# Kernel optimization log

Hardware: AMD Instinct MI355X
Metric: run time of the kernel (lower is better)

Reference implementation:

```python
import math
import jax, jax.numpy as jnp
import numpy as np

D = 256      # embedding_dim (= internal_dim, downsample_rate 1)
H = 8        # num_heads
HD = D // H  # head_dim = 32
NTC = 16     # num_text_classes
NIMG = 4096  # image tokens (64x64)
N = NIMG + NTC
B = 2
NKE = 64     # num_k_exclude_rope


def _rope(x, freqs):
    # x: (b, h, n, c); freqs: (n, c//2, 2) = (cos, sin) of complex rotary factors
    b, h, n, c = x.shape
    xp = x.reshape(b, h, n, c // 2, 2)
    cos, sin = freqs[..., 0], freqs[..., 1]
    xr, xi = xp[..., 0], xp[..., 1]
    out_r = xr * cos - xi * sin
    out_i = xr * sin + xi * cos
    return jnp.stack([out_r, out_i], axis=-1).reshape(b, h, n, c)


def _sep_heads(x):
    b, n, c = x.shape
    return x.reshape(b, n, H, c // H).transpose(0, 2, 1, 3)  # (b,h,n,hd)


def setup_inputs() -> dict:
    key = jax.random.key(0)
    ks = jax.random.split(key, 14)
    s = 0.02
    # rotary factors: unit-norm cos/sin pairs
    ang_img = jax.random.uniform(ks[3], (NIMG, HD // 2)) * (2.0 * np.pi)
    ang_txt = jax.random.uniform(ks[4], (NTC, HD // 2)) * (2.0 * np.pi)
    return {
        "q": jax.random.normal(ks[0], (B, N, D), dtype=jnp.float32),
        "k": jax.random.normal(ks[1], (B, N, D), dtype=jnp.float32),
        "v": jax.random.normal(ks[2], (B, N, D), dtype=jnp.float32),
        "freqs_cis_img": jnp.stack([jnp.cos(ang_img), jnp.sin(ang_img)], axis=-1),
        "freqs_cis_txt": jnp.stack([jnp.cos(ang_txt), jnp.sin(ang_txt)], axis=-1),
        "Wq": jax.random.normal(ks[5], (D, D), dtype=jnp.float32) * s,
        "bq": jnp.zeros((D,), dtype=jnp.float32),
        "Wk": jax.random.normal(ks[6], (D, D), dtype=jnp.float32) * s,
        "bk": jnp.zeros((D,), dtype=jnp.float32),
        "Wv": jax.random.normal(ks[7], (D, D), dtype=jnp.float32) * s,
        "bv": jnp.zeros((D,), dtype=jnp.float32),
        "Wo": jax.random.normal(ks[8], (D, D), dtype=jnp.float32) * s,
        "bo": jnp.zeros((D,), dtype=jnp.float32),
        "num_k_exclude_rope": NKE,
    }


def reference(q, k, v, freqs_cis_img, freqs_cis_txt,
              Wq, bq, Wk, bk, Wv, bv, Wo, bo, num_k_exclude_rope):
    q = q @ Wq.T + bq
    k = k @ Wk.T + bk
    v = v @ Wv.T + bv
    q = _sep_heads(q)  # (b,h,n,hd)
    k = _sep_heads(k)
    v = _sep_heads(v)

    # split tokens into image / text regions, apply RoPE separately
    q_img, q_txt = q[:, :, :-NTC, :], q[:, :, -NTC:, :]
    k_img, k_txt = k[:, :, :-NTC, :], k[:, :, -NTC:, :]
    q_img = _rope(q_img, freqs_cis_img)
    k_img = _rope(k_img, freqs_cis_img)
    q_txt = _rope(q_txt, freqs_cis_txt)
    k_txt = _rope(k_txt, freqs_cis_txt)
    q = jnp.concatenate([q_img, q_txt], axis=-2)
    k = jnp.concatenate([k_img, k_txt], axis=-2)

    scale = 1.0 / math.sqrt(HD)
    nke = num_k_exclude_rope
    if nke > 0:
        k_td, k_mem = k[:, :, :-nke, :], k[:, :, -nke:, :]
        v_td, v_mem = v[:, :, :-nke, :], v[:, :, -nke:, :]
        attn = jax.nn.softmax(jnp.einsum('bhqd,bhkd->bhqk', q, k_td) * scale, axis=-1)
        out = jnp.einsum('bhqk,bhkd->bhqd', attn, v_td)
        attn_m = jax.nn.softmax(jnp.einsum('bhqd,bhkd->bhqk', q, k_mem) * scale, axis=-1)
        out = out + jnp.einsum('bhqk,bhkd->bhqd', attn_m, v_mem)
    else:
        attn = jax.nn.softmax(jnp.einsum('bhqd,bhkd->bhqk', q, k) * scale, axis=-1)
        out = jnp.einsum('bhqk,bhkd->bhqd', attn, v)

    b, h, n, hd = out.shape
    out = out.transpose(0, 2, 1, 3).reshape(b, n, h * hd)
    return out @ Wo.T + bo
```

## Files before the change

kernel.cpp:

```cpp
#include <hip/hip_runtime.h>
#include <hip/hip_bf16.h>

#define BN    4112
#define NKR   4160
#define BNP   4160
#define BB    2
#define HH    8
#define NIMG_ 4096
#define NMAIN 4048
#define MROWS 8224
#define QSCALE 0.25505402f

typedef __attribute__((ext_vector_type(8))) short short8;
typedef __attribute__((ext_vector_type(4))) float f32x4;

__device__ __forceinline__ unsigned short f2bs(float x) { return __bfloat16_as_ushort(__float2bfloat16(x)); }
__device__ __forceinline__ unsigned pkbf(float a, float b) {
    __hip_bfloat162 h = __float22bfloat162_rn(make_float2(a, b));
    unsigned u; __builtin_memcpy(&u, &h, 4); return u;
}
__device__ __forceinline__ float fexp2(float x) {
#if __has_builtin(__builtin_amdgcn_exp2f)
    return __builtin_amdgcn_exp2f(x);
#else
    return exp2f(x);
#endif
}

__global__ __launch_bounds__(256)
void qkv_mfma(const float* __restrict__ Aq, const float* __restrict__ Ak, const float* __restrict__ Av,
              const float* __restrict__ Wq, const float* __restrict__ Wk, const float* __restrict__ Wv,
              const float* __restrict__ bq, const float* __restrict__ bk, const float* __restrict__ bv,
              short* __restrict__ Qr, short* __restrict__ Kr, short* __restrict__ Vt,
              const float* __restrict__ fimg, const float* __restrict__ ftxt)
{
    __shared__ __align__(16) short Ws[2][64][72];
    __shared__ __align__(16) short Ds[2][64][72];

    const int mode = blockIdx.z;
    const float* A    = (mode == 0) ? Aq : (mode == 1) ? Ak : Av;
    const float* W    = (mode == 0) ? Wq : (mode == 1) ? Wk : Wv;
    const float* bias = (mode == 0) ? bq : (mode == 1) ? bk : bv;

    const int t    = threadIdx.x;
    const int wave = t >> 6, lane = t & 63, q16 = lane & 15, quad = lane >> 4;
    const int f0 = blockIdx.x * 64;
    const int m0 = blockIdx.y * 64;
    const int sr = t >> 2, sc = (t & 3) * 16;
    const int arow = m0 + sr;
    const bool aval = arow < MROWS;
    const float* wp = W + (size_t)(f0 + sr) * 256 + sc;
    const float* ap = A + (size_t)(aval ? arow : 0) * 256 + sc;

    f32x4 acc[4] = {{0,0,0,0},{0,0,0,0},{0,0,0,0},{0,0,0,0}};

    uint4 wr0, wr1, dr0, dr1;
    {
        float4 a0 = *(const float4*)(wp),     a1 = *(const float4*)(wp + 4);
        float4 a2 = *(const float4*)(wp + 8), a3 = *(const float4*)(wp + 12);
        wr0 = uint4{pkbf(a0.x,a0.y), pkbf(a0.z,a0.w), pkbf(a1.x,a1.y), pkbf(a1.z,a1.w)};
        wr1 = uint4{pkbf(a2.x,a2.y), pkbf(a2.z,a2.w), pkbf(a3.x,a3.y), pkbf(a3.z,a3.w)};
        a0 = *(const float4*)(ap);     a1 = *(const float4*)(ap + 4);
        a2 = *(const float4*)(ap + 8); a3 = *(const float4*)(ap + 12);
        dr0 = uint4{pkbf(a0.x,a0.y), pkbf(a0.z,a0.w), pkbf(a1.x,a1.y), pkbf(a1.z,a1.w)};
        dr1 = uint4{pkbf(a2.x,a2.y), pkbf(a2.z,a2.w), pkbf(a3.x,a3.y), pkbf(a3.z,a3.w)};
    }
    *(uint4*)&Ws[0][sr][sc] = wr0; *(uint4*)&Ws[0][sr][sc + 8] = wr1;
    *(uint4*)&Ds[0][sr][sc] = dr0; *(uint4*)&Ds[0][sr][sc + 8] = dr1;
    __syncthreads();

    #pragma unroll
    for (int ki = 0; ki < 4; ++ki) {
        const int buf = ki & 1;
        if (ki < 3) {
            const int k1 = (ki + 1) * 64;
            float4 a0 = *(const float4*)(wp + k1),     a1 = *(const float4*)(wp + k1 + 4);
            float4 a2 = *(const float4*)(wp + k1 + 8), a3 = *(const float4*)(wp + k1 + 12);
            wr0 = uint4{pkbf(a0.x,a0.y), pkbf(a0.z,a0.w), pkbf(a1.x,a1.y), pkbf(a1.z,a1.w)};
            wr1 = uint4{pkbf(a2.x,a2.y), pkbf(a2.z,a2.w), pkbf(a3.x,a3.y), pkbf(a3.z,a3.w)};
            a0 = *(const float4*)(ap + k1);     a1 = *(const float4*)(ap + k1 + 4);
            a2 = *(const float4*)(ap + k1 + 8); a3 = *(const float4*)(ap + k1 + 12);
            dr0 = uint4{pkbf(a0.x,a0.y), pkbf(a0.z,a0.w), pkbf(a1.x,a1.y), pkbf(a1.z,a1.w)};
            dr1 = uint4{pkbf(a2.x,a2.y), pkbf(a2.z,a2.w), pkbf(a3.x,a3.y), pkbf(a3.z,a3.w)};
        }
        #pragma unroll
        for (int ks = 0; ks < 2; ++ks) {
            const short8 af = *(const short8*)&Ws[buf][wave * 16 + q16][ks * 32 + quad * 8];
            #pragma unroll
            for (int ct = 0; ct < 4; ++ct) {
                const short8 bf = *(const short8*)&Ds[buf][ct * 16 + q16][ks * 32 + quad * 8];
                acc[ct] = __builtin_amdgcn_mfma_f32_16x16x32_bf16(af, bf, acc[ct], 0, 0, 0);
            }
        }
        if (ki < 3) {
            *(uint4*)&Ws[buf ^ 1][sr][sc] = wr0; *(uint4*)&Ws[buf ^ 1][sr][sc + 8] = wr1;
            *(uint4*)&Ds[buf ^ 1][sr][sc] = dr0; *(uint4*)&Ds[buf ^ 1][sr][sc + 8] = dr1;
            __syncthreads();
        }
    }

    const int fbase = f0 + wave * 16 + quad * 4;
    const float4 bb = *(const float4*)(bias + fbase);
    float vs[4][4];
    #pragma unroll
    for (int ct = 0; ct < 4; ++ct) {
        int n = m0 + ct * 16 + q16;
        float v0 = acc[ct][0] + bb.x, v1 = acc[ct][1] + bb.y;
        float v2 = acc[ct][2] + bb.z, v3 = acc[ct][3] + bb.w;
        int b  = (n >= BN) ? 1 : 0;
        int nb = n - b * BN;
        if (mode < 2) {
            int j0 = (fbase & 31) >> 1;
            const float* fr = (nb < NIMG_) ? (fimg + ((size_t)nb * 16 + j0) * 2)
                                           : (ftxt + ((size_t)(nb - NIMG_) * 16 + j0) * 2);
            float4 cs = *(const float4*)fr;
            float r0 = v0 * cs.x - v1 * cs.y, i0 = v0 * cs.y + v1 * cs.x;
            float r1 = v2 * cs.z - v3 * cs.w, i1 = v2 * cs.w + v3 * cs.z;
            v0 = r0; v1 = i0; v2 = r1; v3 = i1;
        }
        if (mode == 2) {
            vs[ct][0] = v0; vs[ct][1] = v1; vs[ct][2] = v2; vs[ct][3] = v3;
            continue;
        }
        if (n >= MROWS) continue;
        const int h = (fbase >> 5) & 7, hd = fbase & 31;
        if (mode == 0) {
            unsigned short* op = (unsigned short*)Qr + (((size_t)(b * HH + h) * BN + nb) * 32 + hd);
            *(uint2*)op = uint2{pkbf(v0 * QSCALE, v1 * QSCALE), pkbf(v2 * QSCALE, v3 * QSCALE)};
        } else {
            int nk = nb + ((nb >= NMAIN) ? 48 : 0);
            unsigned short* op = (unsigned short*)Kr + (((size_t)(b * HH + h) * NKR + nk) * 32 + hd);
            *(uint2*)op = uint2{pkbf(v0, v1), pkbf(v2, v3)};
        }
    }

    if (mode == 2) {
        short (*Tr)[72] = Ds[0];
        const int fl = wave * 16 + quad * 4;
        #pragma unroll
        for (int ct = 0; ct < 4; ++ct) {
            const int nl = ct * 16 + q16;
            Tr[fl + 0][nl] = (short)f2bs(vs[ct][0]);
            Tr[fl + 1][nl] = (short)f2bs(vs[ct][1]);
            Tr[fl + 2][nl] = (short)f2bs(vs[ct][2]);
            Tr[fl + 3][nl] = (short)f2bs(vs[ct][3]);
        }
        __syncthreads();
        const int h0 = (f0 >> 5) & 7;
        #pragma unroll
        for (int ii = 0; ii < 2; ++ii) {
            const int r  = ii * 32 + (t >> 3);
            const int c8 = (t & 7) * 8;
            const int ng = m0 + c8;
            if (ng < MROWS) {
                uint4 val = *(const uint4*)&Tr[r][c8];
                int b  = (ng >= BN) ? 1 : 0;
                int nb = ng - b * BN;
                int nk = nb + ((nb >= NMAIN) ? 48 : 0);
                int h  = h0 + (r >> 5), hd = r & 31;
                unsigned short* op = (unsigned short*)Vt + ((size_t)(b * HH + h) * 32 + hd) * BNP + nk;
                *(uint4*)op = val;
            }
        }
    }

    if (blockIdx.x == 0 && blockIdx.y < 16 && t < 192) {
        const int bh = blockIdx.y;
        if (mode == 1) {
            short* base = Kr + (size_t)bh * NKR * 32 + (size_t)NMAIN * 32;
            *(uint4*)(base + t * 8) = uint4{0u, 0u, 0u, 0u};
        } else if (mode == 2) {
            short* base = Vt + (size_t)bh * 32 * BNP + (size_t)(t / 6) * BNP + NMAIN + (t % 6) * 8;
            *(uint4*)base = uint4{0u, 0u, 0u, 0u};
        }
    }
}

__global__ __launch_bounds__(256)
void attn_mfma(const short* __restrict__ Qr, const short* __restrict__ Kr,
               const short* __restrict__ Vt, unsigned short* __restrict__ AO)
{
    __shared__ __align__(16) short Ks[2][64][40];
    __shared__ __align__(16) short Vs[2][32][72];

    const int t    = threadIdx.x;
    const int wave = t >> 6, lane = t & 63, q16 = lane & 15, quad = lane >> 4;
    const int bh = blockIdx.y;
    const int q  = blockIdx.x * 64 + wave * 16 + q16;
    const int qc = (q < BN) ? q : (BN - 1);
    const short8 qf = *(const short8*)(Qr + ((size_t)bh * BN + qc) * 32 + quad * 8);

    f32x4 oA0 = {0,0,0,0}, oA1 = {0,0,0,0}, oB0 = {0,0,0,0}, oB1 = {0,0,0,0};
    float LA = 0.f, LB = 0.f;

    const int kr = t >> 2, kc = t & 3;
    const int vr = t >> 3, vc = t & 7;
    const short* kg = Kr + (size_t)bh * NKR * 32 + (size_t)kr * 32 + kc * 8;
    const short* vg = Vt + (size_t)bh * 32 * BNP + (size_t)vr * BNP + vc * 8;

    auto tile = [&](int buf, f32x4& o0, f32x4& o1, float& L) {
        float lsum = 0.f;
        #pragma unroll
        for (int g = 0; g < 2; ++g) {
            const short8 kf0 = *(const short8*)&Ks[buf][(2*g)     * 16 + q16][quad * 8];
            const short8 kf1 = *(const short8*)&Ks[buf][(2*g + 1) * 16 + q16][quad * 8];
            f32x4 z = {0,0,0,0};
            f32x4 s0 = __builtin_amdgcn_mfma_f32_16x16x32_bf16(kf0, qf, z, 0, 0, 0);
            f32x4 s1 = __builtin_amdgcn_mfma_f32_16x16x32_bf16(kf1, qf, z, 0, 0, 0);
            float p0 = fexp2(s0[0]), p1 = fexp2(s0[1]), p2 = fexp2(s0[2]), p3 = fexp2(s0[3]);
            float p4 = fexp2(s1[0]), p5 = fexp2(s1[1]), p6 = fexp2(s1[2]), p7 = fexp2(s1[3]);
            lsum += ((p0 + p1) + (p2 + p3)) + ((p4 + p5) + (p6 + p7));
            uint4 pbu = uint4{pkbf(p0, p1), pkbf(p2, p3), pkbf(p4, p5), pkbf(p6, p7)};
            short8 pb; __builtin_memcpy(&pb, &pbu, 16);
            uint2 va0 = uint2{*(const unsigned*)&Vs[buf][q16][g*32 + quad*4],
                              *(const unsigned*)&Vs[buf][q16][g*32 + quad*4 + 2]};
            uint2 va1 = uint2{*(const unsigned*)&Vs[buf][q16][g*32 + 16 + quad*4],
                              *(const unsigned*)&Vs[buf][q16][g*32 + 16 + quad*4 + 2]};
            uint4 vau = uint4{va0.x, va0.y, va1.x, va1.y};
            short8 vf; __builtin_memcpy(&vf, &vau, 16);
            o0 = __builtin_amdgcn_mfma_f32_16x16x32_bf16(vf, pb, o0, 0, 0, 0);
            uint2 vb0 = uint2{*(const unsigned*)&Vs[buf][16 + q16][g*32 + quad*4],
                              *(const unsigned*)&Vs[buf][16 + q16][g*32 + quad*4 + 2]};
            uint2 vb1 = uint2{*(const unsigned*)&Vs[buf][16 + q16][g*32 + 16 + quad*4],
                              *(const unsigned*)&Vs[buf][16 + q16][g*32 + 16 + quad*4 + 2]};
            uint4 vbu = uint4{vb0.x, vb0.y, vb1.x, vb1.y};
            short8 vg2; __builtin_memcpy(&vg2, &vbu, 16);
            o1 = __builtin_amdgcn_mfma_f32_16x16x32_bf16(vg2, pb, o1, 0, 0, 0);
        }
        L += lsum;
    };

    *(uint4*)&Ks[0][kr][kc * 8] = *(const uint4*)(kg);
    *(uint4*)&Vs[0][vr][vc * 8] = *(const uint4*)(vg);
    __syncthreads();

    for (int it = 0; it < 64; ++it) {
        const int buf = it & 1;
        uint4 kreg = *(const uint4*)(kg + (size_t)(it + 1) * 2048);
        uint4 vreg = *(const uint4*)(vg + (it + 1) * 64);
        tile(buf, oA0, oA1, LA);
        *(uint4*)&Ks[buf ^ 1][kr][kc * 8] = kreg;
        *(uint4*)&Vs[buf ^ 1][vr][vc * 8] = vreg;
        __syncthreads();
    }
    tile(0, oB0, oB1, LB);

    LA += __shfl_xor(LA, 16); LA += __shfl_xor(LA, 32);
    LB += __shfl_xor(LB, 16); LB += __shfl_xor(LB, 32);
    LA -= 48.f;

    if (q < BN) {
        const float iA = 1.f / LA, iB = 1.f / LB;
        const int b = bh >> 3, h = bh & 7;
        unsigned short* ap = AO + ((size_t)b * BN + q) * 256 + h * 32;
        float w0[4], w1[4];
        #pragma unroll
        for (int r = 0; r < 4; ++r) {
            w0[r] = oA0[r] * iA + oB0[r] * iB;
            w1[r] = oA1[r] * iA + oB1[r] * iB;
        }
        *(uint2*)(ap + quad * 4)      = uint2{pkbf(w0[0], w0[1]), pkbf(w0[2], w0[3])};
        *(uint2*)(ap + 16 + quad * 4) = uint2{pkbf(w1[0], w1[1]), pkbf(w1[2], w1[3])};
    }
}

__global__ __launch_bounds__(256)
void gemm_out(const unsigned short* __restrict__ A, const float* __restrict__ W,
              const float* __restrict__ bias, float* __restrict__ out)
{
    __shared__ __align__(16) short Ws[2][64][72];
    __shared__ __align__(16) short Ds[2][64][72];
    const int t    = threadIdx.x;
    const int wave = t >> 6, lane = t & 63, q16 = lane & 15, quad = lane >> 4;
    const int f0 = blockIdx.x * 64, m0 = blockIdx.y * 64;
    const int sr = t >> 2, sc = (t & 3) * 16;
    const int arow = m0 + sr;
    const bool aval = arow < MROWS;
    const float* wp = W + (size_t)(f0 + sr) * 256 + sc;
    const unsigned short* ap = A + (size_t)(aval ? arow : 0) * 256 + sc;

    f32x4 acc[4] = {{0,0,0,0},{0,0,0,0},{0,0,0,0},{0,0,0,0}};

    uint4 wr0, wr1, dr0, dr1;
    {
        float4 a0 = *(const float4*)(wp),     a1 = *(const float4*)(wp + 4);
        float4 a2 = *(const float4*)(wp + 8), a3 = *(const float4*)(wp + 12);
        wr0 = uint4{pkbf(a0.x,a0.y), pkbf(a0.z,a0.w), pkbf(a1.x,a1.y), pkbf(a1.z,a1.w)};
        wr1 = uint4{pkbf(a2.x,a2.y), pkbf(a2.z,a2.w), pkbf(a3.x,a3.y), pkbf(a3.z,a3.w)};
        dr0 = *(const uint4*)(ap); dr1 = *(const uint4*)(ap + 8);
    }
    *(uint4*)&Ws[0][sr][sc] = wr0; *(uint4*)&Ws[0][sr][sc + 8] = wr1;
    *(uint4*)&Ds[0][sr][sc] = dr0; *(uint4*)&Ds[0][sr][sc + 8] = dr1;
    __syncthreads();

    #pragma unroll
    for (int ki = 0; ki < 4; ++ki) {
        const int buf = ki & 1;
        if (ki < 3) {
            const int k1 = (ki + 1) * 64;
            float4 a0 = *(const float4*)(wp + k1),     a1 = *(const float4*)(wp + k1 + 4);
            float4 a2 = *(const float4*)(wp + k1 + 8), a3 = *(const float4*)(wp + k1 + 12);
            wr0 = uint4{pkbf(a0.x,a0.y), pkbf(a0.z,a0.w), pkbf(a1.x,a1.y), pkbf(a1.z,a1.w)};
            wr1 = uint4{pkbf(a2.x,a2.y), pkbf(a2.z,a2.w), pkbf(a3.x,a3.y), pkbf(a3.z,a3.w)};
            dr0 = *(const uint4*)(ap + k1); dr1 = *(const uint4*)(ap + k1 + 8);
        }
        #pragma unroll
        for (int ks = 0; ks < 2; ++ks) {
            const short8 af = *(const short8*)&Ws[buf][wave * 16 + q16][ks * 32 + quad * 8];
            #pragma unroll
            for (int ct = 0; ct < 4; ++ct) {
                const short8 bf = *(const short8*)&Ds[buf][ct * 16 + q16][ks * 32 + quad * 8];
                acc[ct] = __builtin_amdgcn_mfma_f32_16x16x32_bf16(af, bf, acc[ct], 0, 0, 0);
            }
        }
        if (ki < 3) {
            *(uint4*)&Ws[buf ^ 1][sr][sc] = wr0; *(uint4*)&Ws[buf ^ 1][sr][sc + 8] = wr1;
            *(uint4*)&Ds[buf ^ 1][sr][sc] = dr0; *(uint4*)&Ds[buf ^ 1][sr][sc + 8] = dr1;
            __syncthreads();
        }
    }

    const int fbase = f0 + wave * 16 + quad * 4;
    const float4 bb = *(const float4*)(bias + fbase);
    #pragma unroll
    for (int ct = 0; ct < 4; ++ct) {
        int n = m0 + ct * 16 + q16;
        if (n >= MROWS) continue;
        float* op = out + (size_t)n * 256 + fbase;
        *(float4*)op = float4{acc[ct][0] + bb.x, acc[ct][1] + bb.y,
                              acc[ct][2] + bb.z, acc[ct][3] + bb.w};
    }
}

extern "C" void kernel_launch(void* const* d_in, const int* in_sizes, int n_in,
                              void* d_out, int out_size, void* d_ws, size_t ws_size,
                              hipStream_t stream)
{
    (void)in_sizes; (void)n_in; (void)out_size; (void)ws_size;
    const float* q    = (const float*)d_in[0];
    const float* k    = (const float*)d_in[1];
    const float* v    = (const float*)d_in[2];
    const float* fimg = (const float*)d_in[3];
    const float* ftxt = (const float*)d_in[4];
    const float* Wq   = (const float*)d_in[5];
    const float* bq   = (const float*)d_in[6];
    const float* Wk   = (const float*)d_in[7];
    const float* bk   = (const float*)d_in[8];
    const float* Wv   = (const float*)d_in[9];
    const float* bv   = (const float*)d_in[10];
    const float* Wo   = (const float*)d_in[11];
    const float* bo   = (const float*)d_in[12];

    char* w = (char*)d_ws;
    short*          Qr = (short*)(w);
    short*          Kr = (short*)(w + 4210688);
    short*          Vt = (short*)(w + 8470528);
    unsigned short* AO = (unsigned short*)(w + 12730368);

    qkv_mfma<<<dim3(4, 129, 3), 256, 0, stream>>>(q, k, v, Wq, Wk, Wv, bq, bk, bv,
                                                  Qr, Kr, Vt, fimg, ftxt);
    attn_mfma<<<dim3(65, 16), 256, 0, stream>>>(Qr, Kr, Vt, AO);
    gemm_out<<<dim3(4, 129), 256, 0, stream>>>(AO, Wo, bo, (float*)d_out);
}
```

Baseline: 207.5 us.

## Split attention KV loop across two wave groups per block

Doubles the attention block to 512 threads. Each of two 4-wave groups processes half of the key/value tiles for the same 64 queries, each with its own double-buffered LDS staging. The two partial sums are then combined through shared memory before the write. This halves the serial KV loop length per query tile to gain latency hiding and wave parallelism, since the grid has only 1040 blocks. The cost is more LDS per block and an extra reduction barrier.

```diff
diff --git a/kernel.cpp b/kernel.cpp
--- a/kernel.cpp
+++ b/kernel.cpp
@@ -176,34 +176,37 @@
     }
 }
 
-__global__ __launch_bounds__(256)
+__global__ __launch_bounds__(512, 8)
 void attn_mfma(const short* __restrict__ Qr, const short* __restrict__ Kr,
                const short* __restrict__ Vt, unsigned short* __restrict__ AO)
 {
-    __shared__ __align__(16) short Ks[2][64][40];
-    __shared__ __align__(16) short Vs[2][32][72];
+    __shared__ __align__(16) short Ks[2][2][64][40];
+    __shared__ __align__(16) short Vs[2][2][32][72];
 
     const int t    = threadIdx.x;
     const int wave = t >> 6, lane = t & 63, q16 = lane & 15, quad = lane >> 4;
+    const int grp  = wave >> 2, w4 = wave & 3;
     const int bh = blockIdx.y;
-    const int q  = blockIdx.x * 64 + wave * 16 + q16;
+    const int q  = blockIdx.x * 64 + w4 * 16 + q16;
     const int qc = (q < BN) ? q : (BN - 1);
     const short8 qf = *(const short8*)(Qr + ((size_t)bh * BN + qc) * 32 + quad * 8);
 
     f32x4 oA0 = {0,0,0,0}, oA1 = {0,0,0,0}, oB0 = {0,0,0,0}, oB1 = {0,0,0,0};
     float LA = 0.f, LB = 0.f;
 
-    const int kr = t >> 2, kc = t & 3;
-    const int vr = t >> 3, vc = t & 7;
-    const short* kg = Kr + (size_t)bh * NKR * 32 + (size_t)kr * 32 + kc * 8;
-    const short* vg = Vt + (size_t)bh * 32 * BNP + (size_t)vr * BNP + vc * 8;
+    const int tg = t & 255;
+    const int kr = tg >> 2, kc = tg & 3;
+    const int vr = tg >> 3, vc = tg & 7;
+    const short* kg = Kr + (size_t)bh * NKR * 32 + (size_t)grp * 65536 + (size_t)kr * 32 + kc * 8;
+    const short* vg = Vt + (size_t)bh * 32 * BNP + (size_t)vr * BNP + grp * 2048 + vc * 8;
+    const int ntiles = 32 + grp;
 
     auto tile = [&](int buf, f32x4& o0, f32x4& o1, float& L) {
         float lsum = 0.f;
         #pragma unroll
         for (int g = 0; g < 2; ++g) {
-            const short8 kf0 = *(const short8*)&Ks[buf][(2*g)     * 16 + q16][quad * 8];
-            const short8 kf1 = *(const short8*)&Ks[buf][(2*g + 1) * 16 + q16][quad * 8];
+            const short8 kf0 = *(const short8*)&Ks[grp][buf][(2*g)     * 16 + q16][quad * 8];
+            const short8 kf1 = *(const short8*)&Ks[grp][buf][(2*g + 1) * 16 + q16][quad * 8];
             f32x4 z = {0,0,0,0};
             f32x4 s0 = __builtin_amdgcn_mfma_f32_16x16x32_bf16(kf0, qf, z, 0, 0, 0);
             f32x4 s1 = __builtin_amdgcn_mfma_f32_16x16x32_bf16(kf1, qf, z, 0, 0, 0);
@@ -212,52 +215,70 @@
             lsum += ((p0 + p1) + (p2 + p3)) + ((p4 + p5) + (p6 + p7));
             uint4 pbu = uint4{pkbf(p0, p1), pkbf(p2, p3), pkbf(p4, p5), pkbf(p6, p7)};
             short8 pb; __builtin_memcpy(&pb, &pbu, 16);
-            uint2 va0 = uint2{*(const unsigned*)&Vs[buf][q16][g*32 + quad*4],
-                              *(const unsigned*)&Vs[buf][q16][g*32 + quad*4 + 2]};
-            uint2 va1 = uint2{*(const unsigned*)&Vs[buf][q16][g*32 + 16 + quad*4],
-                              *(const unsigned*)&Vs[buf][q16][g*32 + 16 + quad*4 + 2]};
-            uint4 vau = uint4{va0.x, va0.y, va1.x, va1.y};
+            uint4 vau = uint4{*(const unsigned*)&Vs[grp][buf][q16][g*32 + quad*4],
+                              *(const unsigned*)&Vs[grp][buf][q16][g*32 + quad*4 + 2],
+                              *(const unsigned*)&Vs[grp][buf][q16][g*32 + 16 + quad*4],
+                              *(const unsigned*)&Vs[grp][buf][q16][g*32 + 16 + quad*4 + 2]};
             short8 vf; __builtin_memcpy(&vf, &vau, 16);
             o0 = __builtin_amdgcn_mfma_f32_16x16x32_bf16(vf, pb, o0, 0, 0, 0);
-            uint2 vb0 = uint2{*(const unsigned*)&Vs[buf][16 + q16][g*32 + quad*4],
-                              *(const unsigned*)&Vs[buf][16 + q16][g*32 + quad*4 + 2]};
-            uint2 vb1 = uint2{*(const unsigned*)&Vs[buf][16 + q16][g*32 + 16 + quad*4],
-                              *(const unsigned*)&Vs[buf][16 + q16][g*32 + 16 + quad*4 + 2]};
-            uint4 vbu = uint4{vb0.x, vb0.y, vb1.x, vb1.y};
-            short8 vg2; __builtin_memcpy(&vg2, &vbu, 16);
-            o1 = __builtin_amdgcn_mfma_f32_16x16x32_bf16(vg2, pb, o1, 0, 0, 0);
+            uint4 vbu = uint4{*(const unsigned*)&Vs[grp][buf][16 + q16][g*32 + quad*4],
+                              *(const unsigned*)&Vs[grp][buf][16 + q16][g*32 + quad*4 + 2],
+                              *(const unsigned*)&Vs[grp][buf][16 + q16][g*32 + 16 + quad*4],
+                              *(const unsigned*)&Vs[grp][buf][16 + q16][g*32 + 16 + quad*4 + 2]};
+            short8 vb; __builtin_memcpy(&vb, &vbu, 16);
+            o1 = __builtin_amdgcn_mfma_f32_16x16x32_bf16(vb, pb, o1, 0, 0, 0);
         }
         L += lsum;
     };
 
-    *(uint4*)&Ks[0][kr][kc * 8] = *(const uint4*)(kg);
-    *(uint4*)&Vs[0][vr][vc * 8] = *(const uint4*)(vg);
+    *(uint4*)&Ks[grp][0][kr][kc * 8] = *(const uint4*)(kg);
+    *(uint4*)&Vs[grp][0][vr][vc * 8] = *(const uint4*)(vg);
     __syncthreads();
 
-    for (int it = 0; it < 64; ++it) {
+    for (int it = 0; it < 33; ++it) {
         const int buf = it & 1;
-        uint4 kreg = *(const uint4*)(kg + (size_t)(it + 1) * 2048);
-        uint4 vreg = *(const uint4*)(vg + (it + 1) * 64);
-        tile(buf, oA0, oA1, LA);
-        *(uint4*)&Ks[buf ^ 1][kr][kc * 8] = kreg;
-        *(uint4*)&Vs[buf ^ 1][vr][vc * 8] = vreg;
+        uint4 kreg, vreg;
+        const bool pre = (it + 1) < ntiles;
+        if (pre) {
+            kreg = *(const uint4*)(kg + (size_t)(it + 1) * 2048);
+            vreg = *(const uint4*)(vg + (it + 1) * 64);
+        }
+        if (it < ntiles) {
+            if (grp == 0) tile(buf, oA0, oA1, LA);
+            else if (it < 32) tile(buf, oA0, oA1, LA);
+            else              tile(buf, oB0, oB1, LB);
+        }
+        if (pre) {
+            *(uint4*)&Ks[grp][buf ^ 1][kr][kc * 8] = kreg;
+            *(uint4*)&Vs[grp][buf ^ 1][vr][vc * 8] = vreg;
+        }
         __syncthreads();
     }
-    tile(0, oB0, oB1, LB);
 
     LA += __shfl_xor(LA, 16); LA += __shfl_xor(LA, 32);
     LB += __shfl_xor(LB, 16); LB += __shfl_xor(LB, 32);
-    LA -= 48.f;
-
-    if (q < BN) {
-        const float iA = 1.f / LA, iB = 1.f / LB;
+
+    float* ex = (float*)&Ks[0][0][0][0];
+    const int slot = (w4 * 64 + lane) * 12;
+    if (grp == 0) {
+        *(f32x4*)(ex + slot)     = oA0;
+        *(f32x4*)(ex + slot + 4) = oA1;
+        ex[slot + 8] = LA;
+    }
+    __syncthreads();
+
+    if (grp == 1 && q < BN) {
+        f32x4 a0 = *(const f32x4*)(ex + slot);
+        f32x4 a1 = *(const f32x4*)(ex + slot + 4);
+        float LT = LA + ex[slot + 8] - 48.f;
+        const float iA = 1.f / LT, iB = 1.f / LB;
         const int b = bh >> 3, h = bh & 7;
         unsigned short* ap = AO + ((size_t)b * BN + q) * 256 + h * 32;
         float w0[4], w1[4];
         #pragma unroll
         for (int r = 0; r < 4; ++r) {
-            w0[r] = oA0[r] * iA + oB0[r] * iB;
-            w1[r] = oA1[r] * iA + oB1[r] * iB;
+            w0[r] = (oA0[r] + a0[r]) * iA + oB0[r] * iB;
+            w1[r] = (oA1[r] + a1[r]) * iA + oB1[r] * iB;
         }
         *(uint2*)(ap + quad * 4)      = uint2{pkbf(w0[0], w0[1]), pkbf(w0[2], w0[3])};
         *(uint2*)(ap + 16 + quad * 4) = uint2{pkbf(w1[0], w1[1]), pkbf(w1[2], w1[3])};
@@ -359,6 +380,6 @@
 
     qkv_mfma<<<dim3(4, 129, 3), 256, 0, stream>>>(q, k, v, Wq, Wk, Wv, bq, bk, bv,
                                                   Qr, Kr, Vt, fimg, ftxt);
-    attn_mfma<<<dim3(65, 16), 256, 0, stream>>>(Qr, Kr, Vt, AO);
+    attn_mfma<<<dim3(65, 16), 512, 0, stream>>>(Qr, Kr, Vt, AO);
     gemm_out<<<dim3(4, 129), 256, 0, stream>>>(AO, Wo, bo, (float*)d_out);
 }
```

Measured after the change: 199.6 us. 3.8% less time.

## Restructure attention to read K/V straight from global with split-K across two waves

Applied to the files above, without the earlier changes.

The QKV kernel now writes V in a pre-swizzled per-32-key chunk layout so the attention kernel can load MFMA operand fragments directly from global memory without LDS staging. The attention kernel uses 128-thread blocks with 32 queries each. The two waves split the key range, each holding register-prefetched K/V fragments, and their partial sums are merged through a small LDS exchange. The aim is to remove the LDS copy and the per-tile barriers and to double the grid size. In exchange it relies on uncoalesced fragment-sized global loads and adds an imbalance from wave 1 also handling the memory-token tail.

```diff
diff --git a/kernel.cpp b/kernel.cpp
--- a/kernel.cpp
+++ b/kernel.cpp
@@ -3,12 +3,12 @@
 
 #define BN    4112
 #define NKR   4160
-#define BNP   4160
 #define BB    2
 #define HH    8
 #define NIMG_ 4096
 #define NMAIN 4048
 #define MROWS 8224
+#define VPH   4160
 #define QSCALE 0.25505402f
 
 typedef __attribute__((ext_vector_type(8))) short short8;
@@ -25,6 +25,9 @@
 #else
     return exp2f(x);
 #endif
+}
+__device__ __forceinline__ f32x4 mfma16(short8 a, short8 b, f32x4 c) {
+    return __builtin_amdgcn_mfma_f32_16x16x32_bf16(a, b, c, 0, 0, 0);
 }
 
 __global__ __launch_bounds__(256)
@@ -89,7 +92,7 @@
             #pragma unroll
             for (int ct = 0; ct < 4; ++ct) {
                 const short8 bf = *(const short8*)&Ds[buf][ct * 16 + q16][ks * 32 + quad * 8];
-                acc[ct] = __builtin_amdgcn_mfma_f32_16x16x32_bf16(af, bf, acc[ct], 0, 0, 0);
+                acc[ct] = mfma16(af, bf, acc[ct]);
             }
         }
         if (ki < 3) {
@@ -153,114 +156,169 @@
             const int c8 = (t & 7) * 8;
             const int ng = m0 + c8;
             if (ng < MROWS) {
-                uint4 val = *(const uint4*)&Tr[r][c8];
                 int b  = (ng >= BN) ? 1 : 0;
                 int nb = ng - b * BN;
-                int nk = nb + ((nb >= NMAIN) ? 48 : 0);
                 int h  = h0 + (r >> 5), hd = r & 31;
-                unsigned short* op = (unsigned short*)Vt + ((size_t)(b * HH + h) * 32 + hd) * BNP + nk;
-                *(uint4*)op = val;
-            }
-        }
-    }
-
-    if (blockIdx.x == 0 && blockIdx.y < 16 && t < 192) {
+                size_t hdbase = ((size_t)(b * HH + h) * 32 + hd) * VPH;
+                #pragma unroll
+                for (int j = 0; j < 2; ++j) {
+                    int nb4 = nb + j * 4;
+                    int nk  = nb4 + ((nb4 >= NMAIN) ? 48 : 0);
+                    int c = nk >> 5, within = nk & 31;
+                    int slot = ((within >> 2) & 3) * 8 + ((within >> 4) & 1) * 4;
+                    uint2 val = *(const uint2*)&Tr[r][c8 + j * 4];
+                    *(uint2*)((unsigned short*)Vt + hdbase + c * 32 + slot) = val;
+                }
+            }
+        }
+    }
+
+    if (blockIdx.x == 0 && blockIdx.y < 16) {
         const int bh = blockIdx.y;
-        if (mode == 1) {
+        if (mode == 1 && t < 192) {
             short* base = Kr + (size_t)bh * NKR * 32 + (size_t)NMAIN * 32;
             *(uint4*)(base + t * 8) = uint4{0u, 0u, 0u, 0u};
         } else if (mode == 2) {
-            short* base = Vt + (size_t)bh * 32 * BNP + (size_t)(t / 6) * BNP + NMAIN + (t % 6) * 8;
-            *(uint4*)base = uint4{0u, 0u, 0u, 0u};
-        }
-    }
-}
-
-__global__ __launch_bounds__(256)
+            for (int i = t; i < 384; i += 256) {
+                int hd = i / 12, u = i % 12;
+                size_t base = ((size_t)bh * 32 + hd) * VPH;
+                int c, slot;
+                if (u < 4) { c = 126; slot = 4 + u * 8; }
+                else       { c = 127; slot = (u - 4) * 4; }
+                *(uint2*)((unsigned short*)Vt + base + c * 32 + slot) = uint2{0u, 0u};
+            }
+        }
+    }
+}
+
+__global__ __launch_bounds__(128, 4)
 void attn_mfma(const short* __restrict__ Qr, const short* __restrict__ Kr,
-               const short* __restrict__ Vt, unsigned short* __restrict__ AO)
+               const short* __restrict__ Vp, unsigned short* __restrict__ AO)
 {
-    __shared__ __align__(16) short Ks[2][64][40];
-    __shared__ __align__(16) short Vs[2][32][72];
-
-    const int t    = threadIdx.x;
+    __shared__ float ex[64][20];
+
+    const int t = threadIdx.x;
     const int wave = t >> 6, lane = t & 63, q16 = lane & 15, quad = lane >> 4;
     const int bh = blockIdx.y;
-    const int q  = blockIdx.x * 64 + wave * 16 + q16;
-    const int qc = (q < BN) ? q : (BN - 1);
-    const short8 qf = *(const short8*)(Qr + ((size_t)bh * BN + qc) * 32 + quad * 8);
-
-    f32x4 oA0 = {0,0,0,0}, oA1 = {0,0,0,0}, oB0 = {0,0,0,0}, oB1 = {0,0,0,0};
-    float LA = 0.f, LB = 0.f;
-
-    const int kr = t >> 2, kc = t & 3;
-    const int vr = t >> 3, vc = t & 7;
-    const short* kg = Kr + (size_t)bh * NKR * 32 + (size_t)kr * 32 + kc * 8;
-    const short* vg = Vt + (size_t)bh * 32 * BNP + (size_t)vr * BNP + vc * 8;
-
-    auto tile = [&](int buf, f32x4& o0, f32x4& o1, float& L) {
-        float lsum = 0.f;
+    const int qb = blockIdx.x * 32;
+    const int q0 = qb + q16, q1 = qb + 16 + q16;
+    const int q0c = (q0 < BN) ? q0 : BN - 1;
+    const int q1c = (q1 < BN) ? q1 : BN - 1;
+    const short8 qf0 = *(const short8*)(Qr + ((size_t)bh * BN + q0c) * 32 + quad * 8);
+    const short8 qf1 = *(const short8*)(Qr + ((size_t)bh * BN + q1c) * 32 + quad * 8);
+
+    const short* kp  = Kr + (size_t)bh * NKR * 32 + (size_t)wave * 65 * 1024 + q16 * 32 + quad * 8;
+    const short* vb  = Vp + (size_t)bh * 32 * VPH + (size_t)wave * 65 * 32 + quad * 8;
+    const short* vp0 = vb + (size_t)q16 * VPH;
+    const short* vp1 = vb + (size_t)(16 + q16) * VPH;
+
+    f32x4 o00 = {0,0,0,0}, o01 = {0,0,0,0}, o10 = {0,0,0,0}, o11 = {0,0,0,0};
+    f32x4 m00 = {0,0,0,0}, m01 = {0,0,0,0}, m10 = {0,0,0,0}, m11 = {0,0,0,0};
+    float LA0 = 0.f, LA1 = 0.f, LB0 = 0.f, LB1 = 0.f;
+
+    const int ng = 65 - wave * 2;
+
+    short8 kc0 = *(const short8*)(kp);
+    short8 kc1 = *(const short8*)(kp + 512);
+    short8 vc0 = *(const short8*)(vp0);
+    short8 vc1 = *(const short8*)(vp1);
+
+    for (int g = 0; g < ng; ++g) {
+        short8 kn0 = kc0, kn1 = kc1, vn0 = vc0, vn1 = vc1;
+        if (g + 1 < ng) {
+            kn0 = *(const short8*)(kp + (g + 1) * 1024);
+            kn1 = *(const short8*)(kp + (g + 1) * 1024 + 512);
+            vn0 = *(const short8*)(vp0 + (g + 1) * 32);
+            vn1 = *(const short8*)(vp1 + (g + 1) * 32);
+        }
+        const f32x4 z = {0,0,0,0};
+        f32x4 s00 = mfma16(kc0, qf0, z), s01 = mfma16(kc0, qf1, z);
+        f32x4 s10 = mfma16(kc1, qf0, z), s11 = mfma16(kc1, qf1, z);
+        float a0 = fexp2(s00[0]), a1 = fexp2(s00[1]), a2 = fexp2(s00[2]), a3 = fexp2(s00[3]);
+        float b0 = fexp2(s10[0]), b1 = fexp2(s10[1]), b2 = fexp2(s10[2]), b3 = fexp2(s10[3]);
+        float c0 = fexp2(s01[0]), c1 = fexp2(s01[1]), c2 = fexp2(s01[2]), c3 = fexp2(s01[3]);
+        float d0 = fexp2(s11[0]), d1 = fexp2(s11[1]), d2 = fexp2(s11[2]), d3 = fexp2(s11[3]);
+        LA0 += ((a0 + a1) + (a2 + a3)) + ((b0 + b1) + (b2 + b3));
+        LA1 += ((c0 + c1) + (c2 + c3)) + ((d0 + d1) + (d2 + d3));
+        uint4 p0u = uint4{pkbf(a0, a1), pkbf(a2, a3), pkbf(b0, b1), pkbf(b2, b3)};
+        uint4 p1u = uint4{pkbf(c0, c1), pkbf(c2, c3), pkbf(d0, d1), pkbf(d2, d3)};
+        short8 pb0, pb1;
+        __builtin_memcpy(&pb0, &p0u, 16); __builtin_memcpy(&pb1, &p1u, 16);
+        o00 = mfma16(vc0, pb0, o00); o01 = mfma16(vc0, pb1, o01);
+        o10 = mfma16(vc1, pb0, o10); o11 = mfma16(vc1, pb1, o11);
+        kc0 = kn0; kc1 = kn1; vc0 = vn0; vc1 = vn1;
+    }
+
+    if (wave == 1) {
+        const short* kpm  = Kr + (size_t)bh * NKR * 32 + (size_t)4096 * 32 + q16 * 32 + quad * 8;
+        const short* vbm  = Vp + (size_t)bh * 32 * VPH + 128 * 32 + quad * 8;
+        const short* vm0  = vbm + (size_t)q16 * VPH;
+        const short* vm1  = vbm + (size_t)(16 + q16) * VPH;
         #pragma unroll
         for (int g = 0; g < 2; ++g) {
-            const short8 kf0 = *(const short8*)&Ks[buf][(2*g)     * 16 + q16][quad * 8];
-            const short8 kf1 = *(const short8*)&Ks[buf][(2*g + 1) * 16 + q16][quad * 8];
-            f32x4 z = {0,0,0,0};
-            f32x4 s0 = __builtin_amdgcn_mfma_f32_16x16x32_bf16(kf0, qf, z, 0, 0, 0);
-            f32x4 s1 = __builtin_amdgcn_mfma_f32_16x16x32_bf16(kf1, qf, z, 0, 0, 0);
-            float p0 = fexp2(s0[0]), p1 = fexp2(s0[1]), p2 = fexp2(s0[2]), p3 = fexp2(s0[3]);
-            float p4 = fexp2(s1[0]), p5 = fexp2(s1[1]), p6 = fexp2(s1[2]), p7 = fexp2(s1[3]);
-            lsum += ((p0 + p1) + (p2 + p3)) + ((p4 + p5) + (p6 + p7));
-            uint4 pbu = uint4{pkbf(p0, p1), pkbf(p2, p3), pkbf(p4, p5), pkbf(p6, p7)};
-            short8 pb; __builtin_memcpy(&pb, &pbu, 16);
-            uint2 va0 = uint2{*(const unsigned*)&Vs[buf][q16][g*32 + quad*4],
-                              *(const unsigned*)&Vs[buf][q16][g*32 + quad*4 + 2]};
-            uint2 va1 = uint2{*(const unsigned*)&Vs[buf][q16][g*32 + 16 + quad*4],
-                              *(const unsigned*)&Vs[buf][q16][g*32 + 16 + quad*4 + 2]};
-            uint4 vau = uint4{va0.x, va0.y, va1.x, va1.y};
-            short8 vf; __builtin_memcpy(&vf, &vau, 16);
-            o0 = __builtin_amdgcn_mfma_f32_16x16x32_bf16(vf, pb, o0, 0, 0, 0);
-            uint2 vb0 = uint2{*(const unsigned*)&Vs[buf][16 + q16][g*32 + quad*4],
-                              *(const unsigned*)&Vs[buf][16 + q16][g*32 + quad*4 + 2]};
-            uint2 vb1 = uint2{*(const unsigned*)&Vs[buf][16 + q16][g*32 + 16 + quad*4],
-                              *(const unsigned*)&Vs[buf][16 + q16][g*32 + 16 + quad*4 + 2]};
-            uint4 vbu = uint4{vb0.x, vb0.y, vb1.x, vb1.y};
-            short8 vg2; __builtin_memcpy(&vg2, &vbu, 16);
-            o1 = __builtin_amdgcn_mfma_f32_16x16x32_bf16(vg2, pb, o1, 0, 0, 0);
-        }
-        L += lsum;
-    };
-
-    *(uint4*)&Ks[0][kr][kc * 8] = *(const uint4*)(kg);
-    *(uint4*)&Vs[0][vr][vc * 8] = *(const uint4*)(vg);
+            short8 k0 = *(const short8*)(kpm + g * 1024);
+            short8 k1 = *(const short8*)(kpm + g * 1024 + 512);
+            short8 v0 = *(const short8*)(vm0 + g * 32);
+            short8 v1 = *(const short8*)(vm1 + g * 32);
+            const f32x4 z = {0,0,0,0};
+            f32x4 s00 = mfma16(k0, qf0, z), s01 = mfma16(k0, qf1, z);
+            f32x4 s10 = mfma16(k1, qf0, z), s11 = mfma16(k1, qf1, z);
+            float a0 = fexp2(s00[0]), a1 = fexp2(s00[1]), a2 = fexp2(s00[2]), a3 = fexp2(s00[3]);
+            float b0 = fexp2(s10[0]), b1 = fexp2(s10[1]), b2 = fexp2(s10[2]), b3 = fexp2(s10[3]);
+            float c0 = fexp2(s01[0]), c1 = fexp2(s01[1]), c2 = fexp2(s01[2]), c3 = fexp2(s01[3]);
+            float d0 = fexp2(s11[0]), d1 = fexp2(s11[1]), d2 = fexp2(s11[2]), d3 = fexp2(s11[3]);
+            LB0 += ((a0 + a1) + (a2 + a3)) + ((b0 + b1) + (b2 + b3));
+            LB1 += ((c0 + c1) + (c2 + c3)) + ((d0 + d1) + (d2 + d3));
+            uint4 p0u = uint4{pkbf(a0, a1), pkbf(a2, a3), pkbf(b0, b1), pkbf(b2, b3)};
+            uint4 p1u = uint4{pkbf(c0, c1), pkbf(c2, c3), pkbf(d0, d1), pkbf(d2, d3)};
+            short8 pb0, pb1;
+            __builtin_memcpy(&pb0, &p0u, 16); __builtin_memcpy(&pb1, &p1u, 16);
+            m00 = mfma16(v0, pb0, m00); m01 = mfma16(v0, pb1, m01);
+            m10 = mfma16(v1, pb0, m10); m11 = mfma16(v1, pb1, m11);
+        }
+    }
+
+    LA0 += __shfl_xor(LA0, 16); LA0 += __shfl_xor(LA0, 32);
+    LA1 += __shfl_xor(LA1, 16); LA1 += __shfl_xor(LA1, 32);
+    LB0 += __shfl_xor(LB0, 16); LB0 += __shfl_xor(LB0, 32);
+    LB1 += __shfl_xor(LB1, 16); LB1 += __shfl_xor(LB1, 32);
+
+    if (wave == 0) {
+        *(f32x4*)&ex[lane][0]  = o00;
+        *(f32x4*)&ex[lane][4]  = o10;
+        *(f32x4*)&ex[lane][8]  = o01;
+        *(f32x4*)&ex[lane][12] = o11;
+        ex[lane][16] = LA0; ex[lane][17] = LA1;
+    }
     __syncthreads();
 
-    for (int it = 0; it < 64; ++it) {
-        const int buf = it & 1;
-        uint4 kreg = *(const uint4*)(kg + (size_t)(it + 1) * 2048);
-        uint4 vreg = *(const uint4*)(vg + (it + 1) * 64);
-        tile(buf, oA0, oA1, LA);
-        *(uint4*)&Ks[buf ^ 1][kr][kc * 8] = kreg;
-        *(uint4*)&Vs[buf ^ 1][vr][vc * 8] = vreg;
-        __syncthreads();
-    }
-    tile(0, oB0, oB1, LB);
-
-    LA += __shfl_xor(LA, 16); LA += __shfl_xor(LA, 32);
-    LB += __shfl_xor(LB, 16); LB += __shfl_xor(LB, 32);
-    LA -= 48.f;
-
-    if (q < BN) {
-        const float iA = 1.f / LA, iB = 1.f / LB;
+    if (wave == 1) {
         const int b = bh >> 3, h = bh & 7;
-        unsigned short* ap = AO + ((size_t)b * BN + q) * 256 + h * 32;
-        float w0[4], w1[4];
-        #pragma unroll
-        for (int r = 0; r < 4; ++r) {
-            w0[r] = oA0[r] * iA + oB0[r] * iB;
-            w1[r] = oA1[r] * iA + oB1[r] * iB;
-        }
-        *(uint2*)(ap + quad * 4)      = uint2{pkbf(w0[0], w0[1]), pkbf(w0[2], w0[3])};
-        *(uint2*)(ap + 16 + quad * 4) = uint2{pkbf(w1[0], w1[1]), pkbf(w1[2], w1[3])};
+        const float iA0 = 1.f / (LA0 + ex[lane][16] - 48.f);
+        const float iA1 = 1.f / (LA1 + ex[lane][17] - 48.f);
+        const float iB0 = 1.f / LB0, iB1 = 1.f / LB1;
+        if (q0 < BN) {
+            unsigned short* ap = AO + ((size_t)b * BN + q0) * 256 + h * 32;
+            float w0[4], w1[4];
+            #pragma unroll
+            for (int r = 0; r < 4; ++r) {
+                w0[r] = (o00[r] + ex[lane][r])     * iA0 + m00[r] * iB0;
+                w1[r] = (o10[r] + ex[lane][4 + r]) * iA0 + m10[r] * iB0;
+            }
+            *(uint2*)(ap + quad * 4)      = uint2{pkbf(w0[0], w0[1]), pkbf(w0[2], w0[3])};
+            *(uint2*)(ap + 16 + quad * 4) = uint2{pkbf(w1[0], w1[1]), pkbf(w1[2], w1[3])};
+        }
+        if (q1 < BN) {
+            unsigned short* ap = AO + ((size_t)b * BN + q1) * 256 + h * 32;
+            float w0[4], w1[4];
+            #pragma unroll
+            for (int r = 0; r < 4; ++r) {
+                w0[r] = (o01[r] + ex[lane][8 + r])  * iA1 + m01[r] * iB1;
+                w1[r] = (o11[r] + ex[lane][12 + r]) * iA1 + m11[r] * iB1;
+            }
+            *(uint2*)(ap + quad * 4)      = uint2{pkbf(w0[0], w0[1]), pkbf(w0[2], w0[3])};
+            *(uint2*)(ap + 16 + quad * 4) = uint2{pkbf(w1[0], w1[1]), pkbf(w1[2], w1[3])};
+        }
     }
 }
 
@@ -310,7 +368,7 @@
             #pragma unroll
             for (int ct = 0; ct < 4; ++ct) {
                 const short8 bf = *(const short8*)&Ds[buf][ct * 16 + q16][ks * 32 + quad * 8];
-                acc[ct] = __builtin_amdgcn_mfma_f32_16x16x32_bf16(af, bf, acc[ct], 0, 0, 0);
+                acc[ct] = mfma16(af, bf, acc[ct]);
             }
         }
         if (ki < 3) {
@@ -354,11 +412,11 @@
     char* w = (char*)d_ws;
     short*          Qr = (short*)(w);
     short*          Kr = (short*)(w + 4210688);
-    short*          Vt = (short*)(w + 8470528);
+    short*          Vp = (short*)(w + 8470528);
     unsigned short* AO = (unsigned short*)(w + 12730368);
 
     qkv_mfma<<<dim3(4, 129, 3), 256, 0, stream>>>(q, k, v, Wq, Wk, Wv, bq, bk, bv,
-                                                  Qr, Kr, Vt, fimg, ftxt);
-    attn_mfma<<<dim3(65, 16), 256, 0, stream>>>(Qr, Kr, Vt, AO);
+                                                  Qr, Kr, Vp, fimg, ftxt);
+    attn_mfma<<<dim3(129, 16), 128, 0, stream>>>(Qr, Kr, Vp, AO);
     gemm_out<<<dim3(4, 129), 256, 0, stream>>>(AO, Wo, bo, (float*)d_out);
 }
```

New measurement: 224.8 us. +8.3%, slower.
